# Kernel tuning notes

Hardware: AMD Instinct MI355X
Metric: run time of the kernel (lower is better)

The kernel has to match this reference:

```python
import jax, jax.numpy as jnp
import numpy as np

B, K_MAIN, D = 2048, 511, 64


def setup_inputs() -> dict:
    key = jax.random.key(0)
    ks = jax.random.split(key, 8)
    return {
        "vals": jax.random.uniform(ks[0], (B, K_MAIN, D), dtype=jnp.float32),
        "log_density": jax.random.normal(ks[1], (K_MAIN, D), dtype=jnp.float32),
        "logits": jax.random.normal(ks[2], (K_MAIN, D), dtype=jnp.float32),
        "beta_raw": jax.random.normal(ks[3], (K_MAIN,), dtype=jnp.float32),
        "null_vals": jax.random.uniform(ks[4], (B,), dtype=jnp.float32),
        "null_log_density": jax.random.normal(ks[5], (D,), dtype=jnp.float32),
        "null_logits": jax.random.normal(ks[6], (D,), dtype=jnp.float32),
        "null_beta_raw": jax.random.normal(ks[7], (1,), dtype=jnp.float32),
    }


def reference(vals, log_density, logits, beta_raw, null_vals,
              null_log_density, null_logits, null_beta_raw):
    # MenuElement.weights = softmax(logits) per element; beta = clamp(softplus, 0, 10)
    weights = jax.nn.softmax(logits, axis=1)                      # (K_main, D)
    betas = jnp.clip(jax.nn.softplus(beta_raw), 0.0, 10.0)        # (K_main,)
    ld = jnp.clip(log_density, -10.0, 0.0)                        # (K_main, D)
    log_weights = jnp.log(weights + 1e-10) + ld                   # (K_main, D)
    M = jnp.max(log_weights, axis=1, keepdims=True)               # (K_main, 1)
    w_exp = jnp.exp(log_weights - M)                              # (K_main, D)
    # weighted reduction over D for every (valuation b, menu element k)
    weighted_sum = jnp.einsum('bkd,kd->bk', vals, w_exp)          # (B, K_main)
    u_main = jnp.exp(M[:, 0])[None, :] * weighted_sum - betas[None, :]

    # null element
    null_w = jax.nn.softmax(null_logits, axis=0)                  # (D,)
    null_ld = jnp.clip(null_log_density, -10.0, 0.0)
    log_weight_null = jnp.log(null_w + 1e-10) + null_ld           # (D,)
    null_beta = jnp.clip(jax.nn.softplus(null_beta_raw), 0.0, 10.0)[0]
    u_null = jnp.exp(log_weight_null[0]) * null_vals - null_beta  # (B,)

    U = jnp.concatenate([u_main, u_null[:, None]], axis=1)        # (B, K)
    return U
```

## Files before the change

### kernel.cpp

```cpp
#include <hip/hip_runtime.h>
#include <hip/hip_bf16.h>
#include <math.h>

#define B_SZ   2048
#define K_MAIN 511
#define K_OUT  512
#define D_SZ   64

#define WS_COEF  0
#define WS_BETAS (K_MAIN * D_SZ)
#define WS_NULL  (K_MAIN * D_SZ + K_MAIN)

__device__ __forceinline__ float softplus_clip(float x) {
    float sp = (x > 20.f) ? x : log1pf(expf(x));
    return fminf(fmaxf(sp, 0.f), 10.f);
}

__global__ void precompute_kernel(const float* __restrict__ log_density,
                                  const float* __restrict__ logits,
                                  const float* __restrict__ beta_raw,
                                  const float* __restrict__ null_log_density,
                                  const float* __restrict__ null_logits,
                                  const float* __restrict__ null_beta_raw,
                                  float* __restrict__ ws) {
    const int k    = blockIdx.x;
    const int lane = threadIdx.x;

    if (k < K_MAIN) {
        float lg = logits[k * D_SZ + lane];
        float m = lg;
        #pragma unroll
        for (int off = 1; off < 64; off <<= 1) m = fmaxf(m, __shfl_xor(m, off));
        float e = expf(lg - m);
        float s = e;
        #pragma unroll
        for (int off = 1; off < 64; off <<= 1) s += __shfl_xor(s, off);
        float w = e / s;
        float ld = fminf(fmaxf(log_density[k * D_SZ + lane], -10.f), 0.f);
        ws[WS_COEF + k * D_SZ + lane] = (w + 1e-10f) * expf(ld);
        if (lane == 0) {
            ws[WS_BETAS + k] = softplus_clip(beta_raw[k]);
        }
    } else {
        float lg = null_logits[lane];
        float m = lg;
        #pragma unroll
        for (int off = 1; off < 64; off <<= 1) m = fmaxf(m, __shfl_xor(m, off));
        float e = expf(lg - m);
        float s = e;
        #pragma unroll
        for (int off = 1; off < 64; off <<= 1) s += __shfl_xor(s, off);
        if (lane == 0) {
            float w0 = e / s;
            float ld0 = fminf(fmaxf(null_log_density[0], -10.f), 0.f);
            ws[WS_NULL + 0] = (w0 + 1e-10f) * expf(ld0);
            ws[WS_NULL + 1] = softplus_clip(null_beta_raw[0]);
        }
    }
}

__global__ void main_kernel(const float* __restrict__ vals,
                            const float* __restrict__ ws,
                            float* __restrict__ out) {
    const float* __restrict__ coef  = ws + WS_COEF;
    const float* __restrict__ betas = ws + WS_BETAS;

    const unsigned tid     = blockIdx.x * blockDim.x + threadIdx.x;
    const unsigned lane    = threadIdx.x & 63u;
    const unsigned wave    = tid >> 6;
    const unsigned nwaves  = (gridDim.x * blockDim.x) >> 6;
    const unsigned sub     = lane >> 4;
    const unsigned d0      = (lane & 15u) << 2;

    const unsigned total_rows = B_SZ * K_MAIN;
    const unsigned nchunks    = total_rows >> 2;

    for (unsigned chunk = wave; chunk < nchunks; chunk += nwaves) {
        const unsigned row = (chunk << 2) + sub;
        const unsigned k   = row % K_MAIN;
        const unsigned b   = row / K_MAIN;

        const float4 v = *reinterpret_cast<const float4*>(vals + (size_t)row * D_SZ + d0);
        const float4 c = *reinterpret_cast<const float4*>(coef + (size_t)k   * D_SZ + d0);
        float p = v.x * c.x + v.y * c.y + v.z * c.z + v.w * c.w;

        p += __shfl_xor(p, 1);
        p += __shfl_xor(p, 2);
        p += __shfl_xor(p, 4);
        p += __shfl_xor(p, 8);

        if ((lane & 15u) == 0u) {
            out[(size_t)b * K_OUT + k] = p - betas[k];
        }
    }
}

__global__ void null_kernel(const float* __restrict__ null_vals,
                            const float* __restrict__ ws,
                            float* __restrict__ out) {
    const int b = blockIdx.x * blockDim.x + threadIdx.x;
    if (b < B_SZ) {
        out[(size_t)b * K_OUT + K_MAIN] = ws[WS_NULL + 0] * null_vals[b] - ws[WS_NULL + 1];
    }
}

extern "C" void kernel_launch(void* const* d_in, const int* in_sizes, int n_in,
                              void* d_out, int out_size, void* d_ws, size_t ws_size,
                              hipStream_t stream) {
    const float* vals             = (const float*)d_in[0];
    const float* log_density      = (const float*)d_in[1];
    const float* logits           = (const float*)d_in[2];
    const float* beta_raw         = (const float*)d_in[3];
    const float* null_vals        = (const float*)d_in[4];
    const float* null_log_density = (const float*)d_in[5];
    const float* null_logits      = (const float*)d_in[6];
    const float* null_beta_raw    = (const float*)d_in[7];

    float* out = (float*)d_out;
    float* ws  = (float*)d_ws;

    precompute_kernel<<<K_OUT, 64, 0, stream>>>(log_density, logits, beta_raw,
                                                null_log_density, null_logits,
                                                null_beta_raw, ws);

    main_kernel<<<4096, 256, 0, stream>>>(vals, ws, out);

    null_kernel<<<(B_SZ + 255) / 256, 256, 0, stream>>>(null_vals, ws, out);
}
```

Measured before the change: 54.13 us.

## Fuse null-element output into precompute and process two rows per wave iteration

Removes the separate null_kernel launch: the first 32 precompute blocks each recompute the null softmax weight and beta and write 64 null outputs directly. The main kernel now handles two rows per loop iteration per sub-group, issuing two independent vector loads and interleaving their shuffle reductions to raise memory-level parallelism, and gains a launch_bounds hint. The aim is to cut one launch's overhead and hide more load latency, at the cost of redundant null computation across blocks and more registers per thread.

```diff
diff --git a/kernel.cpp b/kernel.cpp
--- a/kernel.cpp
+++ b/kernel.cpp
@@ -9,7 +9,8 @@
 
 #define WS_COEF  0
 #define WS_BETAS (K_MAIN * D_SZ)
-#define WS_NULL  (K_MAIN * D_SZ + K_MAIN)
+
+typedef float f4v __attribute__((ext_vector_type(4)));
 
 __device__ __forceinline__ float softplus_clip(float x) {
     float sp = (x > 20.f) ? x : log1pf(expf(x));
@@ -22,11 +23,13 @@
                                   const float* __restrict__ null_log_density,
                                   const float* __restrict__ null_logits,
                                   const float* __restrict__ null_beta_raw,
-                                  float* __restrict__ ws) {
+                                  const float* __restrict__ null_vals,
+                                  float* __restrict__ ws,
+                                  float* __restrict__ out) {
     const int k    = blockIdx.x;
     const int lane = threadIdx.x;
 
-    if (k < K_MAIN) {
+    {
         float lg = logits[k * D_SZ + lane];
         float m = lg;
         #pragma unroll
@@ -41,7 +44,9 @@
         if (lane == 0) {
             ws[WS_BETAS + k] = softplus_clip(beta_raw[k]);
         }
-    } else {
+    }
+
+    if (k < (B_SZ / 64)) {
         float lg = null_logits[lane];
         float m = lg;
         #pragma unroll
@@ -50,18 +55,19 @@
         float s = e;
         #pragma unroll
         for (int off = 1; off < 64; off <<= 1) s += __shfl_xor(s, off);
-        if (lane == 0) {
-            float w0 = e / s;
-            float ld0 = fminf(fmaxf(null_log_density[0], -10.f), 0.f);
-            ws[WS_NULL + 0] = (w0 + 1e-10f) * expf(ld0);
-            ws[WS_NULL + 1] = softplus_clip(null_beta_raw[0]);
-        }
+        float w0 = expf(null_logits[0] - m) / s;
+        float ld0 = fminf(fmaxf(null_log_density[0], -10.f), 0.f);
+        float c_null = (w0 + 1e-10f) * expf(ld0);
+        float nbeta  = softplus_clip(null_beta_raw[0]);
+        const int b = k * 64 + lane;
+        out[(size_t)b * K_OUT + K_MAIN] = c_null * null_vals[b] - nbeta;
     }
 }
 
-__global__ void main_kernel(const float* __restrict__ vals,
-                            const float* __restrict__ ws,
-                            float* __restrict__ out) {
+__global__ void __launch_bounds__(256)
+main_kernel(const float* __restrict__ vals,
+            const float* __restrict__ ws,
+            float* __restrict__ out) {
     const float* __restrict__ coef  = ws + WS_COEF;
     const float* __restrict__ betas = ws + WS_BETAS;
 
@@ -73,34 +79,35 @@
     const unsigned d0      = (lane & 15u) << 2;
 
     const unsigned total_rows = B_SZ * K_MAIN;
-    const unsigned nchunks    = total_rows >> 2;
+    const unsigned npairs     = total_rows >> 3;
 
-    for (unsigned chunk = wave; chunk < nchunks; chunk += nwaves) {
-        const unsigned row = (chunk << 2) + sub;
-        const unsigned k   = row % K_MAIN;
-        const unsigned b   = row / K_MAIN;
+    for (unsigned p = wave; p < npairs; p += nwaves) {
+        const unsigned row0 = (p << 3) + sub;
+        const unsigned row1 = row0 + 4;
 
-        const float4 v = *reinterpret_cast<const float4*>(vals + (size_t)row * D_SZ + d0);
-        const float4 c = *reinterpret_cast<const float4*>(coef + (size_t)k   * D_SZ + d0);
-        float p = v.x * c.x + v.y * c.y + v.z * c.z + v.w * c.w;
+        const f4v v0 = *reinterpret_cast<const f4v*>(vals + (size_t)row0 * D_SZ + d0);
+        const f4v v1 = *reinterpret_cast<const f4v*>(vals + (size_t)row1 * D_SZ + d0);
 
-        p += __shfl_xor(p, 1);
-        p += __shfl_xor(p, 2);
-        p += __shfl_xor(p, 4);
-        p += __shfl_xor(p, 8);
+        const unsigned k0 = row0 % K_MAIN;
+        const unsigned b0 = row0 / K_MAIN;
+        const unsigned k1 = row1 % K_MAIN;
+        const unsigned b1 = row1 / K_MAIN;
+
+        const f4v c0 = *reinterpret_cast<const f4v*>(coef + (size_t)k0 * D_SZ + d0);
+        const f4v c1 = *reinterpret_cast<const f4v*>(coef + (size_t)k1 * D_SZ + d0);
+
+        float p0 = v0.x * c0.x + v0.y * c0.y + v0.z * c0.z + v0.w * c0.w;
+        float p1 = v1.x * c1.x + v1.y * c1.y + v1.z * c1.z + v1.w * c1.w;
+
+        p0 += __shfl_xor(p0, 1);  p1 += __shfl_xor(p1, 1);
+        p0 += __shfl_xor(p0, 2);  p1 += __shfl_xor(p1, 2);
+        p0 += __shfl_xor(p0, 4);  p1 += __shfl_xor(p1, 4);
+        p0 += __shfl_xor(p0, 8);  p1 += __shfl_xor(p1, 8);
 
         if ((lane & 15u) == 0u) {
-            out[(size_t)b * K_OUT + k] = p - betas[k];
+            out[(size_t)b0 * K_OUT + k0] = p0 - betas[k0];
+            out[(size_t)b1 * K_OUT + k1] = p1 - betas[k1];
         }
-    }
-}
-
-__global__ void null_kernel(const float* __restrict__ null_vals,
-                            const float* __restrict__ ws,
-                            float* __restrict__ out) {
-    const int b = blockIdx.x * blockDim.x + threadIdx.x;
-    if (b < B_SZ) {
-        out[(size_t)b * K_OUT + K_MAIN] = ws[WS_NULL + 0] * null_vals[b] - ws[WS_NULL + 1];
     }
 }
 
@@ -119,11 +126,9 @@
     float* out = (float*)d_out;
     float* ws  = (float*)d_ws;
 
-    precompute_kernel<<<K_OUT, 64, 0, stream>>>(log_density, logits, beta_raw,
-                                                null_log_density, null_logits,
-                                                null_beta_raw, ws);
+    precompute_kernel<<<K_MAIN, 64, 0, stream>>>(log_density, logits, beta_raw,
+                                                 null_log_density, null_logits,
+                                                 null_beta_raw, null_vals, ws, out);
 
     main_kernel<<<4096, 256, 0, stream>>>(vals, ws, out);
-
-    null_kernel<<<(B_SZ + 255) / 256, 256, 0, stream>>>(null_vals, ws, out);
 }
```

Result: faster. 50.28 us (-7.1%).
